# Kernel optimization log

Measured on AMD Instinct MI355X. Metric: run time of the kernel, lower is better.

The kernel has to match this reference:

```python
import jax, jax.numpy as jnp
import numpy as np

BERT = 178  # BERT_VECTOR_SIZE
WLEN = 20   # letters per word (dim1 = WLEN + BERT)


def _lstm(x, h0, c0, Wih, Whh, bih, bhh):
    """PyTorch-convention LSTM (gate order i,f,g,o). x: [B,T,D] -> outputs [B,T,H]."""
    xg = jnp.einsum('btd,gd->btg', x, Wih) + bih + bhh  # precompute input projections

    def step(carry, xt):
        h, c = carry
        g = xt + h @ Whh.T
        i, f, gg, o = jnp.split(g, 4, axis=-1)
        c = jax.nn.sigmoid(f) * c + jax.nn.sigmoid(i) * jnp.tanh(gg)
        h = jax.nn.sigmoid(o) * jnp.tanh(c)
        return (h, c), h

    _, hs = jax.lax.scan(step, (h0, c0), jnp.swapaxes(xg, 0, 1))
    return jnp.swapaxes(hs, 0, 1)  # [B,T,H]


def setup_inputs() -> dict:
    key = jax.random.key(0)
    ks = jax.random.split(key, 32)
    B, S, L = 32, 64, 50          # batch, sentence_length, number_of_letters
    Hs, Hm, D, O = 128, 256, 128, 32  # secondary_hidden, main_hidden, word_dims, output_size
    NW = B * S
    T = WLEN + BERT
    Din = D + BERT                # sentence LSTM input size = 306
    s = 0.05
    rn = lambda k, sh: jax.random.normal(k, sh, dtype=jnp.float32)
    return {
        'X': rn(ks[0], (B, S, T, L)),
        'h0w': rn(ks[1], (NW, Hs)), 'c0w': rn(ks[2], (NW, Hs)),
        'h0f': rn(ks[3], (B, Hm)), 'c0f': rn(ks[4], (B, Hm)),
        'h0b': rn(ks[5], (B, Hm)), 'c0b': rn(ks[6], (B, Hm)),
        'Wih_w': rn(ks[7], (4 * Hs, L)) * s, 'Whh_w': rn(ks[8], (4 * Hs, Hs)) * s,
        'bih_w': rn(ks[9], (4 * Hs,)) * s, 'bhh_w': rn(ks[10], (4 * Hs,)) * s,
        'Wl': rn(ks[11], (D, Hs)) * s, 'bl': rn(ks[12], (D,)) * s,
        'Wih_f': rn(ks[13], (4 * Hm, Din)) * s, 'Whh_f': rn(ks[14], (4 * Hm, Hm)) * s,
        'bih_f': rn(ks[15], (4 * Hm,)) * s, 'bhh_f': rn(ks[16], (4 * Hm,)) * s,
        'Wih_b': rn(ks[17], (4 * Hm, Din)) * s, 'Whh_b': rn(ks[18], (4 * Hm, Hm)) * s,
        'bih_b': rn(ks[19], (4 * Hm,)) * s, 'bhh_b': rn(ks[20], (4 * Hm,)) * s,
        'Wo': rn(ks[21], (O, 2 * Hm)) * s, 'bo': rn(ks[22], (O,)) * s,
    }


def reference(X, h0w, c0w, h0f, c0f, h0b, c0b,
              Wih_w, Whh_w, bih_w, bhh_w, Wl, bl,
              Wih_f, Whh_f, bih_f, bhh_f,
              Wih_b, Whh_b, bih_b, bhh_b, Wo, bo):
    B, S = X.shape[0], X.shape[1]
    L = X.shape[-1]
    NW = B * S
    Xw = X.reshape(NW, -1, L)            # [NW, WLEN+BERT, L]
    letters = Xw[:, :WLEN, :]            # [NW, WLEN, L]
    bert = Xw[:, -BERT:, 0]              # vectorized replacement of the double loop

    out_w = _lstm(letters, h0w, c0w, Wih_w, Whh_w, bih_w, bhh_w)
    word_rep = out_w[:, -1, :] @ Wl.T + bl        # [NW, D]
    word_rep = jnp.concatenate([word_rep, bert], axis=1)  # [NW, D+BERT]
    sentences = word_rep.reshape(B, S, -1)

    out_f = _lstm(sentences, h0f, c0f, Wih_f, Whh_f, bih_f, bhh_f)
    out_b = _lstm(sentences[:, ::-1, :], h0b, c0b, Wih_b, Whh_b, bih_b, bhh_b)[:, ::-1, :]
    out = jnp.concatenate([out_f, out_b], axis=-1)  # [B, S, 2*Hm]

    words = out.reshape(NW, -1)
    tags = words @ Wo.T + bo
    return jax.nn.softmax(tags, axis=1)
```

## Files before the change

### kernel.cpp

```cpp
#include <hip/hip_runtime.h>
#include <cstdint>
#include <cstddef>

#define DI static __device__ __forceinline__

using half_t  = _Float16;
using half2_t = __attribute__((ext_vector_type(2))) _Float16;
using half8_t = __attribute__((ext_vector_type(8))) _Float16;
using f32x4_t = __attribute__((ext_vector_type(4))) float;

DI uint32_t pack2(float a, float b){ half2_t h; h[0]=(half_t)a; h[1]=(half_t)b; return __builtin_bit_cast(uint32_t,h); }
DI uint16_t f16b(float a){ return __builtin_bit_cast(uint16_t,(half_t)a); }
DI float lo16(uint32_t u){ half2_t h=__builtin_bit_cast(half2_t,u); return (float)h[0]; }
DI float hi16(uint32_t u){ half2_t h=__builtin_bit_cast(half2_t,u); return (float)h[1]; }
DI float fdot2(uint32_t w, uint32_t x, float acc){
  return __builtin_amdgcn_fdot2(__builtin_bit_cast(half2_t,w), __builtin_bit_cast(half2_t,x), acc, false);
}
DI float sigm(float x){ return __builtin_amdgcn_rcpf(1.f + __expf(-x)); }
DI float tanhf_(float x){ return 1.f - 2.f*__builtin_amdgcn_rcpf(__expf(2.f*x)+1.f); }

#define SROW 308
#define HSTR 280

#define N0 32768
#define N1 16384
#define N2 8192
#define N3 512
#define N4 262144
#define N5 313344
#define N6 2048
#define N7 8192
#define N8 364544
#define NTOT (N0+N1+N2+N3+N4+N5+N6+N7+N8)

__global__ void k_prep(const float* __restrict__ X,
                       const float* __restrict__ Wih_w, const float* __restrict__ Whh_w,
                       const float* __restrict__ bih_w, const float* __restrict__ bhh_w,
                       const float* __restrict__ Wl,
                       const float* __restrict__ Wih_f, const float* __restrict__ Whh_f,
                       const float* __restrict__ bih_f, const float* __restrict__ bhh_f,
                       const float* __restrict__ Wih_b, const float* __restrict__ Whh_b,
                       const float* __restrict__ bih_b, const float* __restrict__ bhh_b,
                       const float* __restrict__ Wo,
                       uint32_t* __restrict__ wWsw, uint32_t* __restrict__ wWxw,
                       uint32_t* __restrict__ wWlf, float* __restrict__ wbsw,
                       uint32_t* __restrict__ wWs, uint32_t* __restrict__ wWihs,
                       float* __restrict__ wbss, uint32_t* __restrict__ wWo,
                       float* __restrict__ sent)
{
  for (int i = blockIdx.x*blockDim.x + threadIdx.x; i < NTOT; i += gridDim.x*blockDim.x) {
    int id = i;
    if (id < N0) {
      int kp = id & 63, ng = id >> 6;
      int w = ng>>6, g = (ng>>4)&3, jl = ng&15;
      const float* s = Whh_w + (size_t)(g*128 + w*16 + jl)*128 + 2*kp;
      wWsw[id] = pack2(s[0], s[1]);
    } else if ((id -= N0) < N1) {
      int kp = id & 31, ng = id >> 5;
      int w = ng>>6, g = (ng>>4)&3, jl = ng&15;
      if (kp < 25) {
        const float* s = Wih_w + (size_t)(g*128 + w*16 + jl)*50 + 2*kp;
        wWxw[id] = pack2(s[0], s[1]);
      } else wWxw[id] = 0u;
    } else if ((id -= N1) < N2) {
      int kp = id & 63, d = id >> 6;
      const float* s = Wl + (size_t)d*128 + 2*kp;
      wWlf[id] = pack2(s[0], s[1]);
    } else if ((id -= N2) < N3) {
      int g = id & 3, j = id>>2;
      wbsw[id] = bih_w[g*128+j] + bhh_w[g*128+j];
    } else if ((id -= N3) < N4) {
      int kp = id & 127, ng = (id>>7)&1023, dir = id>>17;
      int w = ng>>7, g = (ng>>5)&3, jl = ng&31;
      int row = g*256 + w*32 + jl;
      const float* s = (dir ? Whh_b : Whh_f) + (size_t)row*256 + 2*kp;
      wWs[id] = pack2(s[0], s[1]);
    } else if ((id -= N4) < N5) {
      int dir = id >= 156672; int r = id - dir*156672;
      int g = r & 3, j = (r>>2)&255, kp = r>>10;
      const float* s = (dir ? Wih_b : Wih_f) + (size_t)(g*256+j)*306 + 2*kp;
      wWihs[id] = pack2(s[0], s[1]);
    } else if ((id -= N5) < N6) {
      int g = id & 3, j = (id>>2)&255, dir = id>>10;
      int row = g*256+j;
      wbss[id] = dir ? (bih_b[row]+bhh_b[row]) : (bih_f[row]+bhh_f[row]);
    } else if ((id -= N6) < N7) {
      int o = id & 31, kp = id>>5;
      const float* s = Wo + (size_t)o*512 + 2*kp;
      wWo[id] = pack2(s[0], s[1]);
    } else { id -= N7;
      int wg = id / 178, ii = id % 178;
      sent[(size_t)wg*SROW + 128 + ii] = X[(size_t)wg*9900 + (20+ii)*50];
    }
  }
}

__global__ __launch_bounds__(512, 2) void k_word(
    const float* __restrict__ X, const float* __restrict__ h0w, const float* __restrict__ c0w,
    const uint32_t* __restrict__ wWsw, const uint32_t* __restrict__ wWxw,
    const float* __restrict__ wbsw, const uint32_t* __restrict__ wWlf,
    const float* __restrict__ bl, float* __restrict__ sent)
{
  __shared__ __align__(16) uint32_t lets[11520];
  __shared__ __align__(16) uint16_t hbuf[2][2176];
  const int tid = threadIdx.x;
  const int wave = tid >> 6, lane = tid & 63;
  const int l15 = lane & 15, l4 = lane >> 4;
  const int wg0 = blockIdx.x * 16;

  uint4 Bh[4][4], Bx[4][2];
  #pragma unroll
  for (int g = 0; g < 4; ++g) {
    int ng = wave*64 + g*16 + l15;
    #pragma unroll
    for (int Kt = 0; Kt < 4; ++Kt) Bh[g][Kt] = *(const uint4*)(wWsw + ng*64 + Kt*16 + l4*4);
    #pragma unroll
    for (int Kt = 0; Kt < 2; ++Kt) Bx[g][Kt] = *(const uint4*)(wWxw + ng*32 + Kt*16 + l4*4);
  }
  for (int i = tid; i < 11520; i += 512) {
    int c = i % 36, mt = i / 36; int m = mt & 15, t = mt >> 4;
    lets[i] = (c < 25) ? pack2(X[(size_t)(wg0+m)*9900 + t*50 + 2*c],
                               X[(size_t)(wg0+m)*9900 + t*50 + 2*c + 1]) : 0u;
  }
  for (int i = tid; i < 2048; i += 512) {
    int m = i >> 7, k = i & 127;
    hbuf[0][m*136 + k] = f16b(h0w[(size_t)(wg0+m)*128 + k]);
  }
  const float4 bs = *(const float4*)(wbsw + (wave*16 + l15)*4);
  float cr[4];
  #pragma unroll
  for (int r = 0; r < 4; ++r) cr[r] = c0w[(size_t)(wg0 + l4*4 + r)*128 + wave*16 + l15];
  __syncthreads();

  uint16_t* hc = hbuf[0];
  uint16_t* hn = hbuf[1];
  const uint16_t* lp = (const uint16_t*)lets;
  #pragma unroll 1
  for (int t = 0; t < 20; ++t) {
    f32x4_t acc[4];
    acc[0] = (f32x4_t){bs.x,bs.x,bs.x,bs.x};
    acc[1] = (f32x4_t){bs.y,bs.y,bs.y,bs.y};
    acc[2] = (f32x4_t){bs.z,bs.z,bs.z,bs.z};
    acc[3] = (f32x4_t){bs.w,bs.w,bs.w,bs.w};
    #pragma unroll
    for (int Kt = 0; Kt < 2; ++Kt) {
      uint4 av = *(const uint4*)(lp + (t*16 + l15)*72 + Kt*32 + l4*8);
      half8_t a = __builtin_bit_cast(half8_t, av);
      #pragma unroll
      for (int g = 0; g < 4; ++g)
        acc[g] = __builtin_amdgcn_mfma_f32_16x16x32_f16(a, __builtin_bit_cast(half8_t, Bx[g][Kt]), acc[g], 0,0,0);
    }
    #pragma unroll
    for (int Kt = 0; Kt < 4; ++Kt) {
      uint4 av = *(const uint4*)(hc + l15*136 + Kt*32 + l4*8);
      half8_t a = __builtin_bit_cast(half8_t, av);
      #pragma unroll
      for (int g = 0; g < 4; ++g)
        acc[g] = __builtin_amdgcn_mfma_f32_16x16x32_f16(a, __builtin_bit_cast(half8_t, Bh[g][Kt]), acc[g], 0,0,0);
    }
    #pragma unroll
    for (int r = 0; r < 4; ++r) {
      float cc = sigm(acc[1][r])*cr[r] + sigm(acc[0][r])*tanhf_(acc[2][r]);
      cr[r] = cc;
      float hh = sigm(acc[3][r])*tanhf_(cc);
      hn[(l4*4+r)*136 + wave*16 + l15] = f16b(hh);
    }
    uint16_t* tp = hc; hc = hn; hn = tp;
    __syncthreads();
  }
  uint4 Bl[4];
  #pragma unroll
  for (int Kt = 0; Kt < 4; ++Kt) Bl[Kt] = *(const uint4*)(wWlf + (wave*16 + l15)*64 + Kt*16 + l4*4);
  f32x4_t a2 = (f32x4_t){0.f,0.f,0.f,0.f};
  #pragma unroll
  for (int Kt = 0; Kt < 4; ++Kt) {
    uint4 av = *(const uint4*)(hc + l15*136 + Kt*32 + l4*8);
    a2 = __builtin_amdgcn_mfma_f32_16x16x32_f16(__builtin_bit_cast(half8_t, av),
                                                __builtin_bit_cast(half8_t, Bl[Kt]), a2, 0,0,0);
  }
  const float blv = bl[wave*16 + l15];
  #pragma unroll
  for (int r = 0; r < 4; ++r)
    sent[(size_t)(wg0 + l4*4 + r)*SROW + wave*16 + l15] = a2[r] + blv;
}

__global__ __launch_bounds__(256) void k_sxg(
    const float* __restrict__ sent, const uint32_t* __restrict__ Wihs,
    const float* __restrict__ bss, uint2* __restrict__ xgq)
{
  __shared__ uint32_t x16[153*8];
  const int tid = threadIdx.x;
  const int dir = blockIdx.x >> 8, rg = blockIdx.x & 255;
  for (int i = tid; i < 153*8; i += 256) {
    int r = i & 7, kp = i >> 3;
    int ot = rg*8 + r; int b = ot >> 6, tt = ot & 63;
    int si = dir ? (63 - tt) : tt;
    const float* s = sent + (size_t)(b*64 + si)*SROW + 2*kp;
    x16[kp*8 + r] = pack2(s[0], s[1]);
  }
  __syncthreads();
  const int j = tid;
  float acc[8][4];
  {
    const float4 b4 = *(const float4*)(bss + (dir*256 + j)*4);
    #pragma unroll
    for (int r = 0; r < 8; ++r) { acc[r][0]=b4.x; acc[r][1]=b4.y; acc[r][2]=b4.z; acc[r][3]=b4.w; }
  }
  for (int kp = 0; kp < 153; ++kp) {
    uint4 wv = *(const uint4*)(Wihs + ((size_t)(dir*153 + kp)*256 + j)*4);
    uint4 xa = *(const uint4*)(x16 + kp*8);
    uint4 xb = *(const uint4*)(x16 + kp*8 + 4);
    uint32_t wa[4] = {wv.x,wv.y,wv.z,wv.w};
    uint32_t xs[8] = {xa.x,xa.y,xa.z,xa.w,xb.x,xb.y,xb.z,xb.w};
    #pragma unroll
    for (int r = 0; r < 8; ++r)
      #pragma unroll
      for (int g = 0; g < 4; ++g) acc[r][g] = fdot2(wa[g], xs[r], acc[r][g]);
  }
  const int w = j >> 5, jh2 = (j >> 4) & 1, l15j = j & 15;
  #pragma unroll
  for (int r = 0; r < 8; ++r) {
    int ot = rg*8 + r; int b = ot >> 6, tt = ot & 63;
    int half = b >> 4, l4m = (b >> 2) & 3, rm = b & 3;
    uint2 v; v.x = pack2(acc[r][0], acc[r][1]); v.y = pack2(acc[r][2], acc[r][3]);
    size_t idx = ((((size_t)(dir*64 + tt)*2 + half)*8 + w)*2 + jh2)*256 + l15j*16 + l4m*4 + rm;
    xgq[idx] = v;
  }
}

__global__ __launch_bounds__(512, 2) void k_srec(
    const uint32_t* __restrict__ Ws, const float* __restrict__ h0f, const float* __restrict__ c0f,
    const float* __restrict__ h0b, const float* __restrict__ c0b,
    const uint2* __restrict__ xgq, uint16_t* __restrict__ outfb)
{
  extern __shared__ char smem[];
  uint16_t* h16a = (uint16_t*)(smem + 131072);
  uint16_t* h16b = h16a + 16*HSTR;
  const int tid = threadIdx.x;
  const int wave = tid >> 6, lane = tid & 63;
  const int dir = blockIdx.x >> 1, half = blockIdx.x & 1, m0 = half * 16;
  const int l15 = lane & 15, l4 = lane >> 4;

  uint4 Breg[8][6];
  #pragma unroll
  for (int Nt = 0; Nt < 8; ++Nt) {
    #pragma unroll
    for (int Kt = 0; Kt < 8; ++Kt) {
      int ng = wave*128 + Nt*16 + l15;
      uint4 v = *(const uint4*)(Ws + (size_t)(dir*1024 + ng)*128 + Kt*16 + l4*4);
      if (Kt < 6) Breg[Nt][Kt] = v;
      else *(uint4*)(smem + (((wave*16 + Nt*2 + (Kt-6))*64 + lane)*16)) = v;
    }
  }
  {
    const float* h0 = dir ? h0b : h0f;
    for (int i = tid; i < 16*256; i += 512) {
      int m = i >> 8, k = i & 255;
      h16a[m*HSTR + k] = f16b(h0[(size_t)(m0+m)*256 + k]);
    }
  }
  float cr[2][4];
  {
    const float* c0 = dir ? c0b : c0f;
    #pragma unroll
    for (int jh = 0; jh < 2; ++jh)
      #pragma unroll
      for (int r = 0; r < 4; ++r)
        cr[jh][r] = c0[(size_t)(m0 + l4*4 + r)*256 + wave*32 + jh*16 + l15];
  }
  __syncthreads();

  const char* xbase = (const char*)xgq + (size_t)dir*4194304 + half*32768;
  const uint32_t xlane = wave*4096 + l15*128 + l4*32;
  const int s0 = dir ? 63 : 0;
  const int sdelta = dir ? -65536 : 65536;
  const char* obase = (const char*)outfb + (size_t)s0*65536 + half*32768 + dir*16384;
  const uint32_t olane = (l4*4)*512 + wave*64 + l15*2;
  const uint32_t aoff = l15*HSTR + l4*8;

  uint16_t* hc = h16a;
  uint16_t* hn = h16b;

#define UPD1(JH, R, GI, GF, GG, GO) {                                         \
    float eo = __expf(-(GO));                         \
    float ef = __expf(-(GF)), ei = __expf(-(GI)), eg = __expf(-2.f*(GG));     \
    float pef = 1.f + ef, pei = 1.f + ei, peg = 1.f + eg;                     \
    float num = cr[JH][R]*pei*peg + (1.f - eg)*pef;                           \
    float cc  = num * __builtin_amdgcn_rcpf(pef*pei*peg);                     \
    cr[JH][R] = cc;                                                           \
    float ec = __expf(-2.f*cc);                                               \
    float hh = (1.f - ec) * __builtin_amdgcn_rcpf((1.f + ec)*(1.f + eo));     \
    uint16_t hb = f16b(hh);                                                   \
    hn[(l4*4+(R))*HSTR + wave*32 + (JH)*16 + l15] = hb;                       \
    *(uint16_t*)(obase + olane + (R)*512 + (JH)*32) = hb;                     \
  }

  uint4 p0 = *(const uint4*)(xbase + xlane);
  uint4 p1 = *(const uint4*)(xbase + xlane + 16);
  uint4 p2 = *(const uint4*)(xbase + xlane + 2048);
  uint4 p3 = *(const uint4*)(xbase + xlane + 2064);

  #pragma unroll 1
  for (int t = 0; t < 64; ++t) {
    f32x4_t acc[8];
    acc[0] = (f32x4_t){lo16(p0.x), lo16(p0.z), lo16(p1.x), lo16(p1.z)};
    acc[2] = (f32x4_t){hi16(p0.x), hi16(p0.z), hi16(p1.x), hi16(p1.z)};
    acc[4] = (f32x4_t){lo16(p0.y), lo16(p0.w), lo16(p1.y), lo16(p1.w)};
    acc[6] = (f32x4_t){hi16(p0.y), hi16(p0.w), hi16(p1.y), hi16(p1.w)};
    acc[1] = (f32x4_t){lo16(p2.x), lo16(p2.z), lo16(p3.x), lo16(p3.z)};
    acc[3] = (f32x4_t){hi16(p2.x), hi16(p2.z), hi16(p3.x), hi16(p3.z)};
    acc[5] = (f32x4_t){lo16(p2.y), lo16(p2.w), lo16(p3.y), lo16(p3.w)};
    acc[7] = (f32x4_t){hi16(p2.y), hi16(p2.w), hi16(p3.y), hi16(p3.w)};

    __builtin_amdgcn_s_setprio(1);
    #pragma unroll
    for (int Kt = 0; Kt < 8; ++Kt) {
      uint4 av = *(const uint4*)(hc + aoff + Kt*32);
      half8_t a = __builtin_bit_cast(half8_t, av);
      #pragma unroll
      for (int g = 0; g < 4; ++g) {
        const int Nt = g*2;
        uint4 bv;
        if (Kt < 6) bv = Breg[Nt][Kt];
        else bv = *(const uint4*)(smem + (((wave*16 + Nt*2 + (Kt-6))*64 + lane)*16));
        acc[Nt] = __builtin_amdgcn_mfma_f32_16x16x32_f16(a, __builtin_bit_cast(half8_t, bv), acc[Nt], 0,0,0);
      }
    }
    __builtin_amdgcn_s_setprio(0);

    #pragma unroll
    for (int Kt = 0; Kt < 8; ++Kt) {
      uint4 av = *(const uint4*)(hc + aoff + Kt*32);
      half8_t a = __builtin_bit_cast(half8_t, av);
      #pragma unroll
      for (int g = 0; g < 4; ++g) {
        const int Nt = g*2 + 1;
        uint4 bv;
        if (Kt < 6) bv = Breg[Nt][Kt];
        else bv = *(const uint4*)(smem + (((wave*16 + Nt*2 + (Kt-6))*64 + lane)*16));
        acc[Nt] = __builtin_amdgcn_mfma_f32_16x16x32_f16(a, __builtin_bit_cast(half8_t, bv), acc[Nt], 0,0,0);
      }
      if (Kt & 1) {
        const int r = Kt >> 1;
        UPD1(0, r, acc[0][r], acc[2][r], acc[4][r], acc[6][r]);
        __builtin_amdgcn_sched_group_barrier(0x008, 8, 0);
        __builtin_amdgcn_sched_group_barrier(0x002, 44, 0);
      }
    }

    p0 = *(const uint4*)(xbase + xlane + 65536);
    p1 = *(const uint4*)(xbase + xlane + 65536 + 16);
    p2 = *(const uint4*)(xbase + xlane + 65536 + 2048);
    p3 = *(const uint4*)(xbase + xlane + 65536 + 2064);

    #pragma unroll
    for (int r = 0; r < 4; ++r)
      UPD1(1, r, acc[1][r], acc[3][r], acc[5][r], acc[7][r]);

    { uint16_t* tp = hc; hc = hn; hn = tp; }
    xbase += 65536;
    obase += sdelta;
    asm volatile("s_waitcnt lgkmcnt(0)\ns_barrier" ::: "memory");
  }
#undef UPD1
}

__global__ __launch_bounds__(256) void k_tags(
    const uint16_t* __restrict__ outfb, const uint32_t* __restrict__ Wo16,
    const float* __restrict__ bo, float* __restrict__ out)
{
  __shared__ uint32_t xr[8*256];
  const int tid = threadIdx.x;
  const int w0 = blockIdx.x * 8;
  const uint32_t* src = (const uint32_t*)outfb;
  for (int i = tid; i < 2048; i += 256) {
    int w = i >> 8, kp = i & 255;
    int widx = w0 + w;
    int s = widx & 63, q = widx >> 6;
    int half = q >> 4, m = q & 15;
    int dir = kp >> 7, wv = (kp >> 4) & 7, jh = (kp >> 3) & 1, l15h = kp & 7;
    xr[i] = src[s*16384 + half*8192 + dir*4096 + m*128 + wv*16 + jh*8 + l15h];
  }
  __syncthreads();
  const int o = tid & 31, w = tid >> 5;
  float a = bo[o];
  for (int kp = 0; kp < 256; ++kp)
    a = fdot2(Wo16[kp*32 + o], xr[w*256 + kp], a);
  float mx = a;
  #pragma unroll
  for (int off = 16; off; off >>= 1) mx = fmaxf(mx, __shfl_xor(mx, off, 32));
  float e = __expf(a - mx);
  float ssum = e;
  #pragma unroll
  for (int off = 16; off; off >>= 1) ssum += __shfl_xor(ssum, off, 32);
  out[(size_t)(w0+w)*32 + o] = e * __builtin_amdgcn_rcpf(ssum);
}

extern "C" void kernel_launch(void* const* d_in, const int* in_sizes, int n_in,
                              void* d_out, int out_size, void* d_ws, size_t ws_size,
                              hipStream_t stream) {
  const float* X     = (const float*)d_in[0];
  const float* h0w   = (const float*)d_in[1];
  const float* c0w   = (const float*)d_in[2];
  const float* h0f   = (const float*)d_in[3];
  const float* c0f   = (const float*)d_in[4];
  const float* h0b   = (const float*)d_in[5];
  const float* c0b   = (const float*)d_in[6];
  const float* Wih_w = (const float*)d_in[7];
  const float* Whh_w = (const float*)d_in[8];
  const float* bih_w = (const float*)d_in[9];
  const float* bhh_w = (const float*)d_in[10];
  const float* Wl    = (const float*)d_in[11];
  const float* bl    = (const float*)d_in[12];
  const float* Wih_f = (const float*)d_in[13];
  const float* Whh_f = (const float*)d_in[14];
  const float* bih_f = (const float*)d_in[15];
  const float* bhh_f = (const float*)d_in[16];
  const float* Wih_b = (const float*)d_in[17];
  const float* Whh_b = (const float*)d_in[18];
  const float* bih_b = (const float*)d_in[19];
  const float* bhh_b = (const float*)d_in[20];
  const float* Wo    = (const float*)d_in[21];
  const float* bo    = (const float*)d_in[22];

  char* ws = (char*)d_ws;
  uint32_t* wWsw  = (uint32_t*)(ws + 0);
  uint32_t* wWxw  = (uint32_t*)(ws + 131072);
  uint32_t* wWlf  = (uint32_t*)(ws + 196608);
  float*    wbsw  = (float*)   (ws + 229376);
  uint32_t* wWs   = (uint32_t*)(ws + 231424);
  uint32_t* wWihs = (uint32_t*)(ws + 1280000);
  float*    wbss  = (float*)   (ws + 2533376);
  uint32_t* wWo   = (uint32_t*)(ws + 2541568);
  float*    sent  = (float*)   (ws + 2574336);
  uint2*    xgq   = (uint2*)   (ws + 5097472);
  uint16_t* outfb = (uint16_t*)(ws + 13486080);

  hipFuncSetAttribute((const void*)k_srec, hipFuncAttributeMaxDynamicSharedMemorySize, 148992);

  k_prep<<<2048, 256, 0, stream>>>(X, Wih_w, Whh_w, bih_w, bhh_w, Wl, Wih_f, Whh_f, bih_f, bhh_f,
                                   Wih_b, Whh_b, bih_b, bhh_b, Wo,
                                   wWsw, wWxw, wWlf, wbsw, wWs, wWihs, wbss, wWo, sent);
  k_word<<<128, 512, 0, stream>>>(X, h0w, c0w, wWsw, wWxw, wbsw, wWlf, bl, sent);
  k_sxg<<<512, 256, 0, stream>>>(sent, wWihs, wbss, xgq);
  k_srec<<<4, 512, 148992, stream>>>(wWs, h0f, c0f, h0b, c0b, xgq, outfb);
  k_tags<<<256, 256, 0, stream>>>(outfb, wWo, bo, (float*)d_out);
}
```

Baseline: 306.3 us.

## Use MFMA for sentence input projection and move BERT gather into word kernel

The sentence-LSTM input projection kernel switches from per-thread fdot2 loops to 16x16x32 f16 MFMA tiles, one block per (direction, timestep) covering all 32 batch rows. The input-weight prep is relaid out in padded, MFMA-B-fragment order to match. The BERT-column gather moves from the prep kernel into the word kernel, shrinking prep work. The new kernel reads B fragments straight from global memory with K padded from 153 to 160 pairs.

```diff
diff --git a/kernel.cpp b/kernel.cpp
--- a/kernel.cpp
+++ b/kernel.cpp
@@ -21,17 +21,17 @@
 
 #define SROW 308
 #define HSTR 280
+#define ASTR 344
 
 #define N0 32768
 #define N1 16384
 #define N2 8192
 #define N3 512
 #define N4 262144
-#define N5 313344
+#define N5 327680
 #define N6 2048
 #define N7 8192
-#define N8 364544
-#define NTOT (N0+N1+N2+N3+N4+N5+N6+N7+N8)
+#define NTOT (N0+N1+N2+N3+N4+N5+N6+N7)
 
 __global__ void k_prep(const float* __restrict__ X,
                        const float* __restrict__ Wih_w, const float* __restrict__ Whh_w,
@@ -45,8 +45,7 @@
                        uint32_t* __restrict__ wWsw, uint32_t* __restrict__ wWxw,
                        uint32_t* __restrict__ wWlf, float* __restrict__ wbsw,
                        uint32_t* __restrict__ wWs, uint32_t* __restrict__ wWihs,
-                       float* __restrict__ wbss, uint32_t* __restrict__ wWo,
-                       float* __restrict__ sent)
+                       float* __restrict__ wbss, uint32_t* __restrict__ wWo)
 {
   for (int i = blockIdx.x*blockDim.x + threadIdx.x; i < NTOT; i += gridDim.x*blockDim.x) {
     int id = i;
@@ -76,21 +75,24 @@
       const float* s = (dir ? Whh_b : Whh_f) + (size_t)row*256 + 2*kp;
       wWs[id] = pack2(s[0], s[1]);
     } else if ((id -= N4) < N5) {
-      int dir = id >= 156672; int r = id - dir*156672;
-      int g = r & 3, j = (r>>2)&255, kp = r>>10;
-      const float* s = (dir ? Wih_b : Wih_f) + (size_t)(g*256+j)*306 + 2*kp;
-      wWihs[id] = pack2(s[0], s[1]);
+      int kp = id % 160; int q = id / 160;
+      int ng = q & 1023, dir = q >> 10;
+      int w = ng>>7, g = (ng>>5)&3, jl = ng&31;
+      int row = g*256 + w*32 + jl;
+      uint32_t v = 0u;
+      if (kp < 153) {
+        const float* s = (dir ? Wih_b : Wih_f) + (size_t)row*306 + 2*kp;
+        v = pack2(s[0], s[1]);
+      }
+      wWihs[id] = v;
     } else if ((id -= N5) < N6) {
       int g = id & 3, j = (id>>2)&255, dir = id>>10;
       int row = g*256+j;
       wbss[id] = dir ? (bih_b[row]+bhh_b[row]) : (bih_f[row]+bhh_f[row]);
-    } else if ((id -= N6) < N7) {
+    } else { id -= N6;
       int o = id & 31, kp = id>>5;
       const float* s = Wo + (size_t)o*512 + 2*kp;
       wWo[id] = pack2(s[0], s[1]);
-    } else { id -= N7;
-      int wg = id / 178, ii = id % 178;
-      sent[(size_t)wg*SROW + 128 + ii] = X[(size_t)wg*9900 + (20+ii)*50];
     }
   }
 }
@@ -117,6 +119,10 @@
     #pragma unroll
     for (int Kt = 0; Kt < 2; ++Kt) Bx[g][Kt] = *(const uint4*)(wWxw + ng*32 + Kt*16 + l4*4);
   }
+  for (int i = tid; i < 16*178; i += 512) {
+    int m = i / 178, ii = i - m*178;
+    sent[(size_t)(wg0+m)*SROW + 128 + ii] = X[(size_t)(wg0+m)*9900 + (20+ii)*50];
+  }
   for (int i = tid; i < 11520; i += 512) {
     int c = i % 36, mt = i / 36; int m = mt & 15, t = mt >> 4;
     lets[i] = (c < 25) ? pack2(X[(size_t)(wg0+m)*9900 + t*50 + 2*c],
@@ -184,48 +190,63 @@
     sent[(size_t)(wg0 + l4*4 + r)*SROW + wave*16 + l15] = a2[r] + blv;
 }
 
-__global__ __launch_bounds__(256) void k_sxg(
+__global__ __launch_bounds__(512) void k_sxg(
     const float* __restrict__ sent, const uint32_t* __restrict__ Wihs,
     const float* __restrict__ bss, uint2* __restrict__ xgq)
 {
-  __shared__ uint32_t x16[153*8];
+  __shared__ __align__(16) uint16_t xs[32*ASTR];
   const int tid = threadIdx.x;
-  const int dir = blockIdx.x >> 8, rg = blockIdx.x & 255;
-  for (int i = tid; i < 153*8; i += 256) {
-    int r = i & 7, kp = i >> 3;
-    int ot = rg*8 + r; int b = ot >> 6, tt = ot & 63;
-    int si = dir ? (63 - tt) : tt;
-    const float* s = sent + (size_t)(b*64 + si)*SROW + 2*kp;
-    x16[kp*8 + r] = pack2(s[0], s[1]);
+  const int wave = tid >> 6, lane = tid & 63;
+  const int l15 = lane & 15, l4 = lane >> 4;
+  const int dir = blockIdx.x >> 6, tt = blockIdx.x & 63;
+  const int si = dir ? (63 - tt) : tt;
+
+  for (int i = tid; i < 32*160; i += 512) {
+    int kp = i % 160, b = i / 160;
+    uint32_t v = 0u;
+    if (kp < 153) {
+      const float* s = sent + (size_t)(b*64 + si)*SROW + 2*kp;
+      v = pack2(s[0], s[1]);
+    }
+    *(uint32_t*)(xs + b*ASTR + 2*kp) = v;
   }
   __syncthreads();
-  const int j = tid;
-  float acc[8][4];
-  {
-    const float4 b4 = *(const float4*)(bss + (dir*256 + j)*4);
-    #pragma unroll
-    for (int r = 0; r < 8; ++r) { acc[r][0]=b4.x; acc[r][1]=b4.y; acc[r][2]=b4.z; acc[r][3]=b4.w; }
-  }
-  for (int kp = 0; kp < 153; ++kp) {
-    uint4 wv = *(const uint4*)(Wihs + ((size_t)(dir*153 + kp)*256 + j)*4);
-    uint4 xa = *(const uint4*)(x16 + kp*8);
-    uint4 xb = *(const uint4*)(x16 + kp*8 + 4);
-    uint32_t wa[4] = {wv.x,wv.y,wv.z,wv.w};
-    uint32_t xs[8] = {xa.x,xa.y,xa.z,xa.w,xb.x,xb.y,xb.z,xb.w};
-    #pragma unroll
-    for (int r = 0; r < 8; ++r)
-      #pragma unroll
-      for (int g = 0; g < 4; ++g) acc[r][g] = fdot2(wa[g], xs[r], acc[r][g]);
-  }
-  const int w = j >> 5, jh2 = (j >> 4) & 1, l15j = j & 15;
-  #pragma unroll
-  for (int r = 0; r < 8; ++r) {
-    int ot = rg*8 + r; int b = ot >> 6, tt = ot & 63;
-    int half = b >> 4, l4m = (b >> 2) & 3, rm = b & 3;
-    uint2 v; v.x = pack2(acc[r][0], acc[r][1]); v.y = pack2(acc[r][2], acc[r][3]);
-    size_t idx = ((((size_t)(dir*64 + tt)*2 + half)*8 + w)*2 + jh2)*256 + l15j*16 + l4m*4 + rm;
-    xgq[idx] = v;
-  }
+
+  f32x4_t acc[2][8];
+  #pragma unroll
+  for (int Nt = 0; Nt < 8; ++Nt) {
+    int g = Nt >> 1, jh = Nt & 1;
+    float bv = bss[(dir*256 + wave*32 + jh*16 + l15)*4 + g];
+    acc[0][Nt] = (f32x4_t){bv,bv,bv,bv};
+    acc[1][Nt] = (f32x4_t){bv,bv,bv,bv};
+  }
+  const uint32_t* Bb = Wihs + (size_t)(dir*1024 + wave*128)*160 + l15*160 + l4*4;
+  #pragma unroll
+  for (int Kt = 0; Kt < 10; ++Kt) {
+    uint4 av0 = *(const uint4*)(xs + l15*ASTR + Kt*32 + l4*8);
+    uint4 av1 = *(const uint4*)(xs + (16 + l15)*ASTR + Kt*32 + l4*8);
+    half8_t a0 = __builtin_bit_cast(half8_t, av0);
+    half8_t a1 = __builtin_bit_cast(half8_t, av1);
+    #pragma unroll
+    for (int Nt = 0; Nt < 8; ++Nt) {
+      uint4 bv = *(const uint4*)(Bb + (size_t)Nt*16*160 + Kt*16);
+      half8_t b = __builtin_bit_cast(half8_t, bv);
+      acc[0][Nt] = __builtin_amdgcn_mfma_f32_16x16x32_f16(a0, b, acc[0][Nt], 0,0,0);
+      acc[1][Nt] = __builtin_amdgcn_mfma_f32_16x16x32_f16(a1, b, acc[1][Nt], 0,0,0);
+    }
+  }
+  #pragma unroll
+  for (int Mt = 0; Mt < 2; ++Mt)
+    #pragma unroll
+    for (int jh = 0; jh < 2; ++jh)
+      #pragma unroll
+      for (int r = 0; r < 4; ++r) {
+        uint2 v;
+        v.x = pack2(acc[Mt][0+jh][r], acc[Mt][2+jh][r]);
+        v.y = pack2(acc[Mt][4+jh][r], acc[Mt][6+jh][r]);
+        size_t idx = ((((size_t)(dir*64 + tt)*2 + Mt)*8 + wave)*2 + jh)*256 + l15*16 + l4*4 + r;
+        xgq[idx] = v;
+      }
 }
 
 __global__ __launch_bounds__(512, 2) void k_srec(
@@ -282,7 +303,7 @@
   uint16_t* hn = h16b;
 
 #define UPD1(JH, R, GI, GF, GG, GO) {                                         \
-    float eo = __expf(-(GO));                         \
+    float eo = __expf(-(GO));                                                 \
     float ef = __expf(-(GF)), ei = __expf(-(GI)), eg = __expf(-2.f*(GG));     \
     float pef = 1.f + ef, pei = 1.f + ei, peg = 1.f + eg;                     \
     float num = cr[JH][R]*pei*peg + (1.f - eg)*pef;                           \
@@ -430,19 +451,19 @@
   float*    wbsw  = (float*)   (ws + 229376);
   uint32_t* wWs   = (uint32_t*)(ws + 231424);
   uint32_t* wWihs = (uint32_t*)(ws + 1280000);
-  float*    wbss  = (float*)   (ws + 2533376);
-  uint32_t* wWo   = (uint32_t*)(ws + 2541568);
-  float*    sent  = (float*)   (ws + 2574336);
-  uint2*    xgq   = (uint2*)   (ws + 5097472);
-  uint16_t* outfb = (uint16_t*)(ws + 13486080);
+  float*    wbss  = (float*)   (ws + 2590720);
+  uint32_t* wWo   = (uint32_t*)(ws + 2598912);
+  float*    sent  = (float*)   (ws + 2631680);
+  uint2*    xgq   = (uint2*)   (ws + 5160960);
+  uint16_t* outfb = (uint16_t*)(ws + 13549568);
 
   hipFuncSetAttribute((const void*)k_srec, hipFuncAttributeMaxDynamicSharedMemorySize, 148992);
 
-  k_prep<<<2048, 256, 0, stream>>>(X, Wih_w, Whh_w, bih_w, bhh_w, Wl, Wih_f, Whh_f, bih_f, bhh_f,
+  k_prep<<<1024, 256, 0, stream>>>(X, Wih_w, Whh_w, bih_w, bhh_w, Wl, Wih_f, Whh_f, bih_f, bhh_f,
                                    Wih_b, Whh_b, bih_b, bhh_b, Wo,
-                                   wWsw, wWxw, wWlf, wbsw, wWs, wWihs, wbss, wWo, sent);
+                                   wWsw, wWxw, wWlf, wbsw, wWs, wWihs, wbss, wWo);
   k_word<<<128, 512, 0, stream>>>(X, h0w, c0w, wWsw, wWxw, wbsw, wWlf, bl, sent);
-  k_sxg<<<512, 256, 0, stream>>>(sent, wWihs, wbss, xgq);
+  k_sxg<<<128, 512, 0, stream>>>(sent, wWihs, wbss, xgq);
   k_srec<<<4, 512, 148992, stream>>>(wWs, h0f, c0f, h0b, c0b, xgq, outfb);
   k_tags<<<256, 256, 0, stream>>>(outfb, wWo, bo, (float*)d_out);
 }
```

Measured after the change: 271.8 us. -11.3%, faster.
